# Kernel optimization log

Measured on AMD Instinct MI355X. Metric: run time of the kernel, lower is better.

The kernel has to match this reference:

```python
import jax, jax.numpy as jnp
import numpy as np

B, T, D = 64, 2048, 256


def setup_inputs() -> dict:
    key = jax.random.key(0)
    k_x, k_len, k_w, k_b, k_a = jax.random.split(key, 5)
    xs = jax.random.normal(k_x, (B, T, D), dtype=jnp.float32)
    # ragged lengths -> prefix mask, mimicking per-sample slicing in the torch loop
    lens = jax.random.randint(k_len, (B,), T // 4, T + 1)
    mask = (jnp.arange(T)[None, :] < lens[:, None]).astype(jnp.int32)
    mask2 = jnp.ones((B, T), dtype=jnp.int32)  # unused by the module
    W = jax.random.normal(k_w, (D, D), dtype=jnp.float32) * (1.0 / np.sqrt(D))
    b = jax.random.normal(k_b, (D,), dtype=jnp.float32) * 0.01
    attn = jax.random.normal(k_a, (D,), dtype=jnp.float32)  # nn.Parameter(D,1) squeezed
    return {"xs": xs, "mask": mask, "mask2": mask2, "W": W, "b": b, "attn": attn}


def reference(xs, mask, mask2, W, b, attn):
    # h = tanh(Linear(x)); torch Linear: x @ W.T + b
    h = jnp.tanh(jnp.einsum("btd,ed->bte", xs, W) + b)          # [B,T,D]
    scores = jnp.einsum("btd,d->bt", h, attn)                    # [B,T]
    valid = mask.astype(bool)
    scores = jnp.where(valid, scores, -jnp.inf)                  # softmax over valid frames only
    w = jax.nn.softmax(scores, axis=1)[..., None]                # [B,T,1]
    mu = jnp.sum(xs * w, axis=1)                                 # [B,D]
    var = jnp.maximum(jnp.sum(xs * xs * w, axis=1) - mu * mu, 1e-5)
    return jnp.concatenate([mu, jnp.sqrt(var)], axis=1)          # [B,2D]
```

## Files before the change

### kernel.cpp

```cpp
#include <hip/hip_runtime.h>
#include <hip/hip_bf16.h>
#include <math.h>

#define PB 64
#define PT 2048
#define PD 256
#define PM (PB * PT)

typedef __bf16 bf16x8 __attribute__((ext_vector_type(8)));
typedef short  s16x8  __attribute__((ext_vector_type(8)));
typedef float  f32x4  __attribute__((ext_vector_type(4)));

__device__ __forceinline__ void split_bf16(float x, short& hi, short& lo) {
    unsigned u = __builtin_bit_cast(unsigned, x);
    hi = (short)(u >> 16);
    float hf = __builtin_bit_cast(float, u & 0xffff0000u);
    float r  = x - hf;
    unsigned v  = __builtin_bit_cast(unsigned, r);
    unsigned rb = v + 0x7fffu + ((v >> 16) & 1u);
    lo = (short)(rb >> 16);
}

__global__ __launch_bounds__(256) void prep_kernel(
    const float* __restrict__ W, short* __restrict__ Whi, short* __restrict__ Wlo)
{
    const int idx = blockIdx.x * 256 + threadIdx.x;
    const int e = idx >> 8;
    const int k = idx & 255;
    short h, l;
    split_bf16(W[idx], h, l);
    const int flat = (((e >> 4) * 8 + (k >> 5)) * 64 + ((k & 31) >> 3) * 16 + (e & 15)) * 8 + (k & 7);
    Whi[flat] = h;
    Wlo[flat] = l;
}

#define SBM 64

__global__ __launch_bounds__(256, 2) void score_kernel(
    const float* __restrict__ xs, const short* __restrict__ Whi,
    const short* __restrict__ Wlo, const float* __restrict__ bias,
    const float* __restrict__ attn, float* __restrict__ scores)
{
    __shared__ short Ahi[4 * 8 * 64 * 8];
    __shared__ short Alo[4 * 8 * 64 * 8];
    __shared__ float sred[4][64];

    const int tid = threadIdx.x;
    const int bm  = blockIdx.x * SBM;

#pragma unroll
    for (int p = 0; p < 8; ++p) {
        const int r  = p * 8 + (tid >> 5);
        const int kb = tid & 31;
        const float4 a0 = *(const float4*)&xs[(bm + r) * PD + kb * 8];
        const float4 a1 = *(const float4*)&xs[(bm + r) * PD + kb * 8 + 4];
        const float f[8] = {a0.x, a0.y, a0.z, a0.w, a1.x, a1.y, a1.z, a1.w};
        s16x8 h, l;
#pragma unroll
        for (int j = 0; j < 8; ++j) { short hh, ll; split_bf16(f[j], hh, ll); h[j] = hh; l[j] = ll; }
        const int mt = r >> 4, m_loc = r & 15;
        const int kt = kb >> 2, quad = kb & 3;
        const int msw = m_loc ^ (kb & 7);
        const int a_idx = (((mt * 8 + kt) * 64) + quad * 16 + msw) * 8;
        *(s16x8*)&Ahi[a_idx] = h;
        *(s16x8*)&Alo[a_idx] = l;
    }
    __syncthreads();

    const int lane = tid & 63;
    const int w    = tid >> 6;
    const int quad = lane >> 4;
    const int nl   = lane & 15;

    f32x4 acc[4][4] = {};

#pragma unroll 2
    for (int kt = 0; kt < 8; ++kt) {
        bf16x8 bh[4], bl[4];
#pragma unroll
        for (int n = 0; n < 4; ++n) {
            const int nt = w * 4 + n;
            const int bidx = ((nt * 8 + kt) * 64 + lane) * 8;
            bh[n] = *(const bf16x8*)&Whi[bidx];
            bl[n] = *(const bf16x8*)&Wlo[bidx];
        }
        s16x8 ah[4], al[4];
        const int msw = nl ^ ((kt * 4 + quad) & 7);
#pragma unroll
        for (int m = 0; m < 4; ++m) {
            const int a_idx = ((m * 8 + kt) * 64 + quad * 16 + msw) * 8;
            ah[m] = *(const s16x8*)&Ahi[a_idx];
            al[m] = *(const s16x8*)&Alo[a_idx];
        }
#pragma unroll
        for (int m = 0; m < 4; ++m) {
            const bf16x8 ahm = __builtin_bit_cast(bf16x8, ah[m]);
            const bf16x8 alm = __builtin_bit_cast(bf16x8, al[m]);
#pragma unroll
            for (int n = 0; n < 4; ++n) {
                acc[m][n] = __builtin_amdgcn_mfma_f32_16x16x32_bf16(ahm, bh[n], acc[m][n], 0, 0, 0);
                acc[m][n] = __builtin_amdgcn_mfma_f32_16x16x32_bf16(ahm, bl[n], acc[m][n], 0, 0, 0);
                acc[m][n] = __builtin_amdgcn_mfma_f32_16x16x32_bf16(alm, bh[n], acc[m][n], 0, 0, 0);
            }
        }
    }

#pragma unroll
    for (int m = 0; m < 4; ++m) {
        float rs[4] = {0.f, 0.f, 0.f, 0.f};
#pragma unroll
        for (int n = 0; n < 4; ++n) {
            const int col = w * 64 + n * 16 + nl;
            const float bv = bias[col];
            const float av = attn[col];
#pragma unroll
            for (int r = 0; r < 4; ++r) {
                const float u  = acc[m][n][r] + bv;
                const float e2 = __expf(2.f * u);
                const float th = 1.f - 2.f * __builtin_amdgcn_rcpf(e2 + 1.f);
                rs[r] = fmaf(th, av, rs[r]);
            }
        }
#pragma unroll
        for (int off = 1; off < 16; off <<= 1) {
#pragma unroll
            for (int r = 0; r < 4; ++r) rs[r] += __shfl_xor(rs[r], off);
        }
        if (nl == 0) {
#pragma unroll
            for (int r = 0; r < 4; ++r) sred[w][m * 16 + quad * 4 + r] = rs[r];
        }
    }
    __syncthreads();
    if (tid < 64)
        scores[bm + tid] = sred[0][tid] + sred[1][tid] + sred[2][tid] + sred[3][tid];
}

__global__ __launch_bounds__(256) void softmax_kernel(
    const int* __restrict__ mask, float* __restrict__ sw)
{
    const int b   = blockIdx.x;
    const int tid = threadIdx.x;
    __shared__ float red[256];

    float s[8];
    int   v[8];
    float mx = -INFINITY;
#pragma unroll
    for (int i = 0; i < 8; ++i) {
        const int t = i * 256 + tid;
        s[i] = sw[b * PT + t];
        v[i] = mask[b * PT + t];
        if (v[i]) mx = fmaxf(mx, s[i]);
    }
    red[tid] = mx;
    __syncthreads();
    for (int st = 128; st > 0; st >>= 1) {
        if (tid < st) red[tid] = fmaxf(red[tid], red[tid + st]);
        __syncthreads();
    }
    mx = red[0];
    __syncthreads();

    float p[8];
    float ls = 0.f;
#pragma unroll
    for (int i = 0; i < 8; ++i) {
        p[i] = v[i] ? __expf(s[i] - mx) : 0.f;
        ls += p[i];
    }
    red[tid] = ls;
    __syncthreads();
    for (int st = 128; st > 0; st >>= 1) {
        if (tid < st) red[tid] += red[tid + st];
        __syncthreads();
    }
    const float inv = 1.f / red[0];
#pragma unroll
    for (int i = 0; i < 8; ++i) sw[b * PT + i * 256 + tid] = p[i] * inv;
}

__global__ __launch_bounds__(256) void moments_kernel(
    const float* __restrict__ xs, const float* __restrict__ w,
    float* __restrict__ part)
{
    const int chunk = blockIdx.x;
    const int b     = blockIdx.y;
    const int tid   = threadIdx.x;
    const int c     = tid & 63;
    const int tq    = tid >> 6;

    __shared__ float  lw[128];
    __shared__ float4 rmu[4][64];
    __shared__ float4 rm2[4][64];

    if (tid < 128) lw[tid] = w[b * PT + chunk * 128 + tid];
    __syncthreads();

    float4 mu = {0.f, 0.f, 0.f, 0.f};
    float4 m2 = {0.f, 0.f, 0.f, 0.f};
    for (int i = 0; i < 32; ++i) {
        const int tl = tq * 32 + i;
        const float wv = lw[tl];
        const float4 x = *(const float4*)&xs[(b * PT + chunk * 128 + tl) * PD + c * 4];
        mu.x = fmaf(wv, x.x, mu.x); mu.y = fmaf(wv, x.y, mu.y);
        mu.z = fmaf(wv, x.z, mu.z); mu.w = fmaf(wv, x.w, mu.w);
        m2.x = fmaf(wv * x.x, x.x, m2.x); m2.y = fmaf(wv * x.y, x.y, m2.y);
        m2.z = fmaf(wv * x.z, x.z, m2.z); m2.w = fmaf(wv * x.w, x.w, m2.w);
    }
    rmu[tq][c] = mu;
    rm2[tq][c] = m2;
    __syncthreads();

    if (tid < 64) {
        float4 smu = rmu[0][tid], sm2 = rm2[0][tid];
        for (int q = 1; q < 4; ++q) {
            const float4 a = rmu[q][tid], d = rm2[q][tid];
            smu.x += a.x; smu.y += a.y; smu.z += a.z; smu.w += a.w;
            sm2.x += d.x; sm2.y += d.y; sm2.z += d.z; sm2.w += d.w;
        }
        const int base = (b * 16 + chunk) * 512;
        *(float4*)&part[base + tid * 4]       = smu;
        *(float4*)&part[base + 256 + tid * 4] = sm2;
    }
}

__global__ __launch_bounds__(256) void finalize_kernel(
    const float* __restrict__ part, float* __restrict__ out)
{
    const int b = blockIdx.x;
    const int d = threadIdx.x;
    float m1 = 0.f, m2 = 0.f;
#pragma unroll
    for (int ch = 0; ch < 16; ++ch) {
        const int base = (b * 16 + ch) * 512;
        m1 += part[base + d];
        m2 += part[base + 256 + d];
    }
    const float var = fmaxf(m2 - m1 * m1, 1e-5f);
    out[b * 512 + d]       = m1;
    out[b * 512 + 256 + d] = sqrtf(var);
}

extern "C" void kernel_launch(void* const* d_in, const int* in_sizes, int n_in,
                              void* d_out, int out_size, void* d_ws, size_t ws_size,
                              hipStream_t stream) {
    const float* xs   = (const float*)d_in[0];
    const int*   mask = (const int*)d_in[1];
    const float* W    = (const float*)d_in[3];
    const float* bias = (const float*)d_in[4];
    const float* attn = (const float*)d_in[5];
    float* out = (float*)d_out;

    float* scores = (float*)d_ws;
    float* part   = scores + PB * PT;
    short* Whi    = (short*)(part + PB * 16 * 512);
    short* Wlo    = Whi + PD * PD;

    prep_kernel<<<PD * PD / 256, 256, 0, stream>>>(W, Whi, Wlo);
    score_kernel<<<PM / SBM, 256, 0, stream>>>(xs, Whi, Wlo, bias, attn, scores);
    softmax_kernel<<<PB, 256, 0, stream>>>(mask, scores);
    moments_kernel<<<dim3(16, PB), 256, 0, stream>>>(xs, scores, part);
    finalize_kernel<<<PB, 256, 0, stream>>>(part, out);
}
```

Baseline: 260.0 us.

## Drop low bf16 half of activations in score GEMM and raise occupancy

The score GEMM now rounds activations to a single bf16 value instead of a hi/lo split, so each K step issues two MFMAs per tile instead of three. The LDS tile for the low half goes away, halving shared memory, and launch bounds rise to allow four blocks per CU. Bias and attention loads are hoisted out of the epilogue loop, and the softmax reductions switch from a shared-memory tree to wave shuffles. Activation precision drops from about fp32-equivalent to bf16 with fp32 weights, which may affect how closely the scores match the reference.

```diff
diff --git a/kernel.cpp b/kernel.cpp
--- a/kernel.cpp
+++ b/kernel.cpp
@@ -11,14 +11,16 @@
 typedef short  s16x8  __attribute__((ext_vector_type(8)));
 typedef float  f32x4  __attribute__((ext_vector_type(4)));
 
+__device__ __forceinline__ short rne_bf16(float x) {
+    unsigned u = __builtin_bit_cast(unsigned, x);
+    return (short)((u + 0x7fffu + ((u >> 16) & 1u)) >> 16);
+}
+
 __device__ __forceinline__ void split_bf16(float x, short& hi, short& lo) {
     unsigned u = __builtin_bit_cast(unsigned, x);
     hi = (short)(u >> 16);
     float hf = __builtin_bit_cast(float, u & 0xffff0000u);
-    float r  = x - hf;
-    unsigned v  = __builtin_bit_cast(unsigned, r);
-    unsigned rb = v + 0x7fffu + ((v >> 16) & 1u);
-    lo = (short)(rb >> 16);
+    lo = rne_bf16(x - hf);
 }
 
 __global__ __launch_bounds__(256) void prep_kernel(
@@ -36,13 +38,12 @@
 
 #define SBM 64
 
-__global__ __launch_bounds__(256, 2) void score_kernel(
+__global__ __launch_bounds__(256, 4) void score_kernel(
     const float* __restrict__ xs, const short* __restrict__ Whi,
     const short* __restrict__ Wlo, const float* __restrict__ bias,
     const float* __restrict__ attn, float* __restrict__ scores)
 {
-    __shared__ short Ahi[4 * 8 * 64 * 8];
-    __shared__ short Alo[4 * 8 * 64 * 8];
+    __shared__ short Ah[4 * 8 * 64 * 8];
     __shared__ float sred[4][64];
 
     const int tid = threadIdx.x;
@@ -55,15 +56,13 @@
         const float4 a0 = *(const float4*)&xs[(bm + r) * PD + kb * 8];
         const float4 a1 = *(const float4*)&xs[(bm + r) * PD + kb * 8 + 4];
         const float f[8] = {a0.x, a0.y, a0.z, a0.w, a1.x, a1.y, a1.z, a1.w};
-        s16x8 h, l;
-#pragma unroll
-        for (int j = 0; j < 8; ++j) { short hh, ll; split_bf16(f[j], hh, ll); h[j] = hh; l[j] = ll; }
+        s16x8 h;
+#pragma unroll
+        for (int j = 0; j < 8; ++j) h[j] = rne_bf16(f[j]);
         const int mt = r >> 4, m_loc = r & 15;
         const int kt = kb >> 2, quad = kb & 3;
         const int msw = m_loc ^ (kb & 7);
-        const int a_idx = (((mt * 8 + kt) * 64) + quad * 16 + msw) * 8;
-        *(s16x8*)&Ahi[a_idx] = h;
-        *(s16x8*)&Alo[a_idx] = l;
+        *(s16x8*)&Ah[(((mt * 8 + kt) * 64) + quad * 16 + msw) * 8] = h;
     }
     __syncthreads();
 
@@ -84,41 +83,40 @@
             bh[n] = *(const bf16x8*)&Whi[bidx];
             bl[n] = *(const bf16x8*)&Wlo[bidx];
         }
-        s16x8 ah[4], al[4];
+        s16x8 ah[4];
         const int msw = nl ^ ((kt * 4 + quad) & 7);
 #pragma unroll
-        for (int m = 0; m < 4; ++m) {
-            const int a_idx = ((m * 8 + kt) * 64 + quad * 16 + msw) * 8;
-            ah[m] = *(const s16x8*)&Ahi[a_idx];
-            al[m] = *(const s16x8*)&Alo[a_idx];
-        }
+        for (int m = 0; m < 4; ++m)
+            ah[m] = *(const s16x8*)&Ah[((m * 8 + kt) * 64 + quad * 16 + msw) * 8];
 #pragma unroll
         for (int m = 0; m < 4; ++m) {
             const bf16x8 ahm = __builtin_bit_cast(bf16x8, ah[m]);
-            const bf16x8 alm = __builtin_bit_cast(bf16x8, al[m]);
 #pragma unroll
             for (int n = 0; n < 4; ++n) {
                 acc[m][n] = __builtin_amdgcn_mfma_f32_16x16x32_bf16(ahm, bh[n], acc[m][n], 0, 0, 0);
                 acc[m][n] = __builtin_amdgcn_mfma_f32_16x16x32_bf16(ahm, bl[n], acc[m][n], 0, 0, 0);
-                acc[m][n] = __builtin_amdgcn_mfma_f32_16x16x32_bf16(alm, bh[n], acc[m][n], 0, 0, 0);
             }
         }
     }
 
+    float bv[4], av[4];
+#pragma unroll
+    for (int n = 0; n < 4; ++n) {
+        const int col = w * 64 + n * 16 + nl;
+        bv[n] = bias[col];
+        av[n] = attn[col];
+    }
 #pragma unroll
     for (int m = 0; m < 4; ++m) {
         float rs[4] = {0.f, 0.f, 0.f, 0.f};
 #pragma unroll
         for (int n = 0; n < 4; ++n) {
-            const int col = w * 64 + n * 16 + nl;
-            const float bv = bias[col];
-            const float av = attn[col];
 #pragma unroll
             for (int r = 0; r < 4; ++r) {
-                const float u  = acc[m][n][r] + bv;
+                const float u  = acc[m][n][r] + bv[n];
                 const float e2 = __expf(2.f * u);
                 const float th = 1.f - 2.f * __builtin_amdgcn_rcpf(e2 + 1.f);
-                rs[r] = fmaf(th, av, rs[r]);
+                rs[r] = fmaf(th, av[n], rs[r]);
             }
         }
 #pragma unroll
@@ -139,9 +137,11 @@
 __global__ __launch_bounds__(256) void softmax_kernel(
     const int* __restrict__ mask, float* __restrict__ sw)
 {
-    const int b   = blockIdx.x;
-    const int tid = threadIdx.x;
-    __shared__ float red[256];
+    const int b    = blockIdx.x;
+    const int tid  = threadIdx.x;
+    const int lane = tid & 63;
+    const int wv   = tid >> 6;
+    __shared__ float wred[4];
 
     float s[8];
     int   v[8];
@@ -153,13 +153,11 @@
         v[i] = mask[b * PT + t];
         if (v[i]) mx = fmaxf(mx, s[i]);
     }
-    red[tid] = mx;
-    __syncthreads();
-    for (int st = 128; st > 0; st >>= 1) {
-        if (tid < st) red[tid] = fmaxf(red[tid], red[tid + st]);
-        __syncthreads();
-    }
-    mx = red[0];
+#pragma unroll
+    for (int off = 1; off < 64; off <<= 1) mx = fmaxf(mx, __shfl_xor(mx, off));
+    if (lane == 0) wred[wv] = mx;
+    __syncthreads();
+    mx = fmaxf(fmaxf(wred[0], wred[1]), fmaxf(wred[2], wred[3]));
     __syncthreads();
 
     float p[8];
@@ -169,13 +167,11 @@
         p[i] = v[i] ? __expf(s[i] - mx) : 0.f;
         ls += p[i];
     }
-    red[tid] = ls;
-    __syncthreads();
-    for (int st = 128; st > 0; st >>= 1) {
-        if (tid < st) red[tid] += red[tid + st];
-        __syncthreads();
-    }
-    const float inv = 1.f / red[0];
+#pragma unroll
+    for (int off = 1; off < 64; off <<= 1) ls += __shfl_xor(ls, off);
+    if (lane == 0) wred[wv] = ls;
+    __syncthreads();
+    const float inv = 1.f / (wred[0] + wred[1] + wred[2] + wred[3]);
 #pragma unroll
     for (int i = 0; i < 8; ++i) sw[b * PT + i * 256 + tid] = p[i] * inv;
 }
```

Result: faster. 252.3 us (-3.0%).
